# Performance work log

Hardware: AMD Instinct MI355X
Metric: run time of the kernel (lower is better)

The kernel has to match this reference:

```python
import jax, jax.numpy as jnp
import numpy as np

B, L, D = 4096, 200, 64


def setup_inputs() -> dict:
    key = jax.random.key(0)
    ks = jax.random.split(key, 7)
    target_key = jax.random.normal(ks[0], (B, D), dtype=jnp.float32)
    item_keys = jax.random.normal(ks[1], (B, L, D), dtype=jnp.float32)
    item_values = jax.random.normal(ks[2], (B, L, D), dtype=jnp.float32)
    mask = jax.random.randint(ks[3], (B, L), 0, 2, dtype=jnp.int32)
    # Linear(D, D, bias=False) weights; torch applies y = x @ W.T
    scale = 1.0 / np.sqrt(D)
    W_target = jax.random.uniform(ks[4], (D, D), jnp.float32, -scale, scale)
    W_item = jax.random.uniform(ks[5], (D, D), jnp.float32, -scale, scale)
    W_value = jax.random.uniform(ks[6], (D, D), jnp.float32, -scale, scale)
    return {
        "target_key": target_key,
        "item_keys": item_keys,
        "item_values": item_values,
        "mask": mask,
        "W_target": W_target,
        "W_item": W_item,
        "W_value": W_value,
    }


def reference(target_key, item_keys, item_values, mask, W_target, W_item, W_value):
    scaler = jnp.float32(D) ** 0.5
    q = target_key @ W_target.T                      # [B, D]
    k = jnp.einsum("bld,ed->ble", item_keys, W_item)   # [B, L, D]
    v = jnp.einsum("bld,ed->ble", item_values, W_value) # [B, L, D]
    # single-query scores: broadcast multiply + reduce over D
    scores = jnp.einsum("bd,bld->bl", q, k) / scaler  # [B, L]
    scores = scores + (-1e8) * (1.0 - mask.astype(scores.dtype))
    w = jax.nn.softmax(scores, axis=1)                # softmax over L
    return jnp.einsum("bl,bld->bd", w, v)             # [B, D]
```

## Files before the change

kernel.cpp:

```cpp
#include <hip/hip_runtime.h>


#define B_ 4096
#define L_ 200
#define D_ 64

__global__ __launch_bounds__(256, 3) void ta_kernel(
    const float* __restrict__ tk,
    const float* __restrict__ ik,
    const float* __restrict__ iv,
    const int*   __restrict__ mask,
    const float* __restrict__ Wt,
    const float* __restrict__ Wi,
    const float* __restrict__ Wv,
    float* __restrict__ out)
{
  const int t = threadIdx.x;
  const int b = blockIdx.x;
  const int c  = t & 15;
  const int rg = t >> 4;

  __shared__ float q_s[D_];
  __shared__ float qt_s[D_];
  __shared__ float bias_s[L_];
  __shared__ float sc[208];
  __shared__ float red[8];
  __shared__ float vred[256 * 4];
  __shared__ float sv[D_];

  if (t < L_) {
    int m = mask[(size_t)b * L_ + t];
    bias_s[t] = m ? 0.0f : -1e8f;
  }

  if (t < D_) {
    const float4* tkb4 = (const float4*)(tk + (size_t)b * D_);
    const float4* Wt4  = (const float4*)Wt;
    float a = 0.f;
#pragma unroll
    for (int j = 0; j < 16; ++j) {
      float4 w = Wt4[t * 16 + j];
      float4 x = tkb4[j];
      a += w.x * x.x + w.y * x.y + w.z * x.z + w.w * x.w;
    }
    q_s[t] = a;
  }
  __syncthreads();
  if (t < D_) {
    float a = 0.f;
#pragma unroll
    for (int e = 0; e < D_; ++e) a += q_s[e] * Wi[e * D_ + t];
    qt_s[t] = a;
  }
  __syncthreads();

  const float4* ik4 = (const float4*)(ik + (size_t)b * (L_ * D_));
  const float4* iv4 = (const float4*)(iv + (size_t)b * (L_ * D_));
  float4 K[13], V[13];
#pragma unroll
  for (int it = 0; it < 12; ++it) K[it] = ik4[it * 256 + t];
  K[12] = (192 + rg < L_) ? ik4[12 * 256 + t] : make_float4(0.f, 0.f, 0.f, 0.f);
#pragma unroll
  for (int it = 0; it < 12; ++it) V[it] = iv4[it * 256 + t];
  V[12] = (192 + rg < L_) ? iv4[12 * 256 + t] : make_float4(0.f, 0.f, 0.f, 0.f);

  const float4 qc = ((const float4*)qt_s)[c];
#pragma unroll
  for (int it = 0; it < 13; ++it) {
    float4 kv = K[it];
    float p = kv.x * qc.x + kv.y * qc.y + kv.z * qc.z + kv.w * qc.w;
    p += __shfl_xor(p, 8, 64);
    p += __shfl_xor(p, 4, 64);
    p += __shfl_xor(p, 2, 64);
    p += __shfl_xor(p, 1, 64);
    int row = it * 16 + rg;
    if (c == 0 && row < L_) sc[row] = p * 0.125f + bias_s[row];
  }
  __syncthreads();

  float v = (t < L_) ? sc[t] : -3.0e38f;
#pragma unroll
  for (int off = 32; off >= 1; off >>= 1)
    v = fmaxf(v, __shfl_xor(v, off, 64));
  if ((t & 63) == 0) red[t >> 6] = v;
  __syncthreads();
  float mx = fmaxf(fmaxf(red[0], red[1]), fmaxf(red[2], red[3]));
  float ex = (t < L_) ? expf(sc[t] - mx) : 0.f;
  float s = ex;
#pragma unroll
  for (int off = 32; off >= 1; off >>= 1)
    s += __shfl_xor(s, off, 64);
  if ((t & 63) == 0) red[4 + (t >> 6)] = s;
  __syncthreads();
  float tot = red[4] + red[5] + red[6] + red[7];
  if (t < L_)      sc[t] = ex / tot;
  else if (t < 208) sc[t] = 0.f;
  __syncthreads();

  float4 acc = make_float4(0.f, 0.f, 0.f, 0.f);
#pragma unroll
  for (int it = 0; it < 13; ++it) {
    float w = sc[it * 16 + rg];
    acc.x += w * V[it].x; acc.y += w * V[it].y;
    acc.z += w * V[it].z; acc.w += w * V[it].w;
  }
  ((float4*)vred)[t] = acc;
  __syncthreads();
  if (t < D_) {
    float a = 0.f;
#pragma unroll
    for (int rg2 = 0; rg2 < 16; ++rg2) a += vred[rg2 * 64 + t];
    sv[t] = a;
  }
  __syncthreads();

  if (t < D_) {
    const float4* Wv4 = (const float4*)Wv;
    const float4* sv4 = (const float4*)sv;
    float a = 0.f;
#pragma unroll
    for (int cc = 0; cc < 16; ++cc) {
      float4 w4 = Wv4[t * 16 + cc];
      float4 s4 = sv4[cc];
      a += w4.x * s4.x + w4.y * s4.y + w4.z * s4.z + w4.w * s4.w;
    }
    out[(size_t)b * D_ + t] = a;
  }
}

extern "C" void kernel_launch(void* const* d_in, const int* in_sizes, int n_in,
                              void* d_out, int out_size, void* d_ws, size_t ws_size,
                              hipStream_t stream) {
  const float* tk   = (const float*)d_in[0];
  const float* ik   = (const float*)d_in[1];
  const float* iv   = (const float*)d_in[2];
  const int*   mask = (const int*)  d_in[3];
  const float* Wt   = (const float*)d_in[4];
  const float* Wi   = (const float*)d_in[5];
  const float* Wv   = (const float*)d_in[6];
  float* out = (float*)d_out;

  ta_kernel<<<B_, 256, 0, stream>>>(tk, ik, iv, mask, Wt, Wi, Wv, out);
}
```

Before: 416.9 us.

## Map one batch row per wavefront with register-window streaming and no shared memory

Each wavefront now handles one batch element (four per block) instead of a whole 256-thread block, and every barrier and LDS buffer is replaced by wave shuffles. K and V are streamed through a rotating 12-entry register window, with sched_barrier pins that keep loads in flight while computing. Softmax normalisation is deferred to the end, and the block's occupancy hint rises. The cost is a serial 50-step loop per wave, so each wave has less memory-level parallelism than the old per-block 13-row prefetch.

```diff
diff --git a/kernel.cpp b/kernel.cpp
--- a/kernel.cpp
+++ b/kernel.cpp
@@ -4,8 +4,11 @@
 #define B_ 4096
 #define L_ 200
 #define D_ 64
+#define WIN 12
 
-__global__ __launch_bounds__(256, 3) void ta_kernel(
+#define PIN() __builtin_amdgcn_sched_barrier(0x387)
+
+__global__ __launch_bounds__(256, 4) void ta_kernel(
     const float* __restrict__ tk,
     const float* __restrict__ ik,
     const float* __restrict__ iv,
@@ -15,117 +18,114 @@
     const float* __restrict__ Wv,
     float* __restrict__ out)
 {
-  const int t = threadIdx.x;
-  const int b = blockIdx.x;
-  const int c  = t & 15;
-  const int rg = t >> 4;
+  const int lane = threadIdx.x & 63;
+  const int b    = blockIdx.x * 4 + (threadIdx.x >> 6);
+  const int c    = lane & 15;
+  const int rg   = lane >> 4;
 
-  __shared__ float q_s[D_];
-  __shared__ float qt_s[D_];
-  __shared__ float bias_s[L_];
-  __shared__ float sc[208];
-  __shared__ float red[8];
-  __shared__ float vred[256 * 4];
-  __shared__ float sv[D_];
+  const float4* tkb4 = (const float4*)(tk + (size_t)b * D_);
+  const float4* Wt4  = (const float4*)Wt;
+  float q = 0.f;
+#pragma unroll
+  for (int j = 0; j < 16; ++j) {
+    float4 w = Wt4[lane * 16 + j];
+    float4 x = tkb4[j];
+    q += w.x * x.x + w.y * x.y + w.z * x.z + w.w * x.w;
+  }
+  float qt = 0.f;
+#pragma unroll
+  for (int e = 0; e < 64; ++e) {
+    float qe = __shfl(q, e, 64);
+    qt += qe * Wi[e * D_ + lane];
+  }
+  float4 qc;
+  qc.x = __shfl(qt, 4 * c + 0, 64);
+  qc.y = __shfl(qt, 4 * c + 1, 64);
+  qc.z = __shfl(qt, 4 * c + 2, 64);
+  qc.w = __shfl(qt, 4 * c + 3, 64);
 
-  if (t < L_) {
-    int m = mask[(size_t)b * L_ + t];
-    bias_s[t] = m ? 0.0f : -1e8f;
+  float bias[4];
+#pragma unroll
+  for (int j = 0; j < 4; ++j) {
+    int r = 64 * j + 4 * c + rg;
+    if (j < 3 || c < 2) {
+      int m = mask[(size_t)b * L_ + r];
+      bias[j] = m ? 0.f : -1e8f;
+    } else {
+      bias[j] = 0.f;
+    }
   }
-
-  if (t < D_) {
-    const float4* tkb4 = (const float4*)(tk + (size_t)b * D_);
-    const float4* Wt4  = (const float4*)Wt;
-    float a = 0.f;
-#pragma unroll
-    for (int j = 0; j < 16; ++j) {
-      float4 w = Wt4[t * 16 + j];
-      float4 x = tkb4[j];
-      a += w.x * x.x + w.y * x.y + w.z * x.z + w.w * x.w;
-    }
-    q_s[t] = a;
-  }
-  __syncthreads();
-  if (t < D_) {
-    float a = 0.f;
-#pragma unroll
-    for (int e = 0; e < D_; ++e) a += q_s[e] * Wi[e * D_ + t];
-    qt_s[t] = a;
-  }
-  __syncthreads();
 
   const float4* ik4 = (const float4*)(ik + (size_t)b * (L_ * D_));
   const float4* iv4 = (const float4*)(iv + (size_t)b * (L_ * D_));
-  float4 K[13], V[13];
+
+  float4 w_[WIN];
 #pragma unroll
-  for (int it = 0; it < 12; ++it) K[it] = ik4[it * 256 + t];
-  K[12] = (192 + rg < L_) ? ik4[12 * 256 + t] : make_float4(0.f, 0.f, 0.f, 0.f);
+  for (int i = 0; i < WIN; ++i) w_[i] = ik4[i * 64 + lane];
+  PIN();
+
+  float s[4] = {-3e38f, -3e38f, -3e38f, -3e38f};
 #pragma unroll
-  for (int it = 0; it < 12; ++it) V[it] = iv4[it * 256 + t];
-  V[12] = (192 + rg < L_) ? iv4[12 * 256 + t] : make_float4(0.f, 0.f, 0.f, 0.f);
-
-  const float4 qc = ((const float4*)qt_s)[c];
-#pragma unroll
-  for (int it = 0; it < 13; ++it) {
-    float4 kv = K[it];
+  for (int it = 0; it < 50; ++it) {
+    float4 kv = w_[it % WIN];
+    if (it + WIN < 50) w_[it % WIN] = ik4[(it + WIN) * 64 + lane];
     float p = kv.x * qc.x + kv.y * qc.y + kv.z * qc.z + kv.w * qc.w;
     p += __shfl_xor(p, 8, 64);
     p += __shfl_xor(p, 4, 64);
     p += __shfl_xor(p, 2, 64);
     p += __shfl_xor(p, 1, 64);
-    int row = it * 16 + rg;
-    if (c == 0 && row < L_) sc[row] = p * 0.125f + bias_s[row];
+    if (c == (it & 15)) s[it >> 4] = p * 0.125f + bias[it >> 4];
+    PIN();
   }
-  __syncthreads();
 
-  float v = (t < L_) ? sc[t] : -3.0e38f;
+#pragma unroll
+  for (int i = 0; i < WIN; ++i) w_[i] = iv4[i * 64 + lane];
+  PIN();
+
+  float mx = fmaxf(fmaxf(s[0], s[1]), fmaxf(s[2], s[3]));
 #pragma unroll
   for (int off = 32; off >= 1; off >>= 1)
-    v = fmaxf(v, __shfl_xor(v, off, 64));
-  if ((t & 63) == 0) red[t >> 6] = v;
-  __syncthreads();
-  float mx = fmaxf(fmaxf(red[0], red[1]), fmaxf(red[2], red[3]));
-  float ex = (t < L_) ? expf(sc[t] - mx) : 0.f;
-  float s = ex;
+    mx = fmaxf(mx, __shfl_xor(mx, off, 64));
+  float e_[4];
+#pragma unroll
+  for (int j = 0; j < 4; ++j) e_[j] = __expf(s[j] - mx);
+  float tt = e_[0] + e_[1] + e_[2] + e_[3];
 #pragma unroll
   for (int off = 32; off >= 1; off >>= 1)
-    s += __shfl_xor(s, off, 64);
-  if ((t & 63) == 0) red[4 + (t >> 6)] = s;
-  __syncthreads();
-  float tot = red[4] + red[5] + red[6] + red[7];
-  if (t < L_)      sc[t] = ex / tot;
-  else if (t < 208) sc[t] = 0.f;
-  __syncthreads();
+    tt += __shfl_xor(tt, off, 64);
+  float rtot = 1.0f / tt;
 
   float4 acc = make_float4(0.f, 0.f, 0.f, 0.f);
 #pragma unroll
-  for (int it = 0; it < 13; ++it) {
-    float w = sc[it * 16 + rg];
-    acc.x += w * V[it].x; acc.y += w * V[it].y;
-    acc.z += w * V[it].z; acc.w += w * V[it].w;
+  for (int it = 0; it < 50; ++it) {
+    float4 vv = w_[it % WIN];
+    if (it + WIN < 50) w_[it % WIN] = iv4[(it + WIN) * 64 + lane];
+    float wgt = __shfl(e_[it >> 4], (lane & 48) | (it & 15), 64);
+    acc.x += wgt * vv.x;
+    acc.y += wgt * vv.y;
+    acc.z += wgt * vv.z;
+    acc.w += wgt * vv.w;
+    PIN();
   }
-  ((float4*)vred)[t] = acc;
-  __syncthreads();
-  if (t < D_) {
-    float a = 0.f;
+
+  acc.x *= rtot; acc.y *= rtot; acc.z *= rtot; acc.w *= rtot;
+  acc.x += __shfl_xor(acc.x, 16, 64); acc.x += __shfl_xor(acc.x, 32, 64);
+  acc.y += __shfl_xor(acc.y, 16, 64); acc.y += __shfl_xor(acc.y, 32, 64);
+  acc.z += __shfl_xor(acc.z, 16, 64); acc.z += __shfl_xor(acc.z, 32, 64);
+  acc.w += __shfl_xor(acc.w, 16, 64); acc.w += __shfl_xor(acc.w, 32, 64);
+
+  const float4* Wv4 = (const float4*)Wv;
+  float o = 0.f;
 #pragma unroll
-    for (int rg2 = 0; rg2 < 16; ++rg2) a += vred[rg2 * 64 + t];
-    sv[t] = a;
+  for (int c2 = 0; c2 < 16; ++c2) {
+    float sx = __shfl(acc.x, c2, 64);
+    float sy = __shfl(acc.y, c2, 64);
+    float sz = __shfl(acc.z, c2, 64);
+    float sw = __shfl(acc.w, c2, 64);
+    float4 w4 = Wv4[lane * 16 + c2];
+    o += sx * w4.x + sy * w4.y + sz * w4.z + sw * w4.w;
   }
-  __syncthreads();
-
-  if (t < D_) {
-    const float4* Wv4 = (const float4*)Wv;
-    const float4* sv4 = (const float4*)sv;
-    float a = 0.f;
-#pragma unroll
-    for (int cc = 0; cc < 16; ++cc) {
-      float4 w4 = Wv4[t * 16 + cc];
-      float4 s4 = sv4[cc];
-      a += w4.x * s4.x + w4.y * s4.y + w4.z * s4.z + w4.w * s4.w;
-    }
-    out[(size_t)b * D_ + t] = a;
-  }
+  out[(size_t)b * D_ + lane] = o;
 }
 
 extern "C" void kernel_launch(void* const* d_in, const int* in_sizes, int n_in,
@@ -140,5 +140,5 @@
   const float* Wv   = (const float*)d_in[6];
   float* out = (float*)d_out;
 
-  ta_kernel<<<B_, 256, 0, stream>>>(tk, ik, iv, mask, Wt, Wi, Wv, out);
+  ta_kernel<<<B_ / 4, 256, 0, stream>>>(tk, ik, iv, mask, Wt, Wi, Wv, out);
 }
```

Result: slower. 429.8 us (+3.1%).
